# Optimization experiments

Hardware: AMD Instinct MI355X
Metric: run time of the kernel (lower is better)

The kernel has to match this reference:

```python
import jax, jax.numpy as jnp
import numpy as np

THETA = 10000.0
NUM_HEADS = 16


def _rope(x, token_positions):
    # x: [B, H, S, d_k], token_positions: [B, S]
    d_k = x.shape[-1]
    half = d_k // 2
    k = jnp.arange(half, dtype=jnp.float32)
    inv_k = THETA ** (-2.0 * k / d_k)                      # [half]
    pos = token_positions.astype(jnp.float32)              # [B, S]
    angles = pos[..., None] * inv_k                         # [B, S, half]
    angles = jnp.repeat(angles, 2, axis=-1)                 # [B, S, d_k] interleaved
    cos = jnp.cos(angles)[:, None]                          # [B, 1, S, d_k]
    sin = jnp.sin(angles)[:, None]
    x_even = x[..., ::2]
    x_odd = x[..., 1::2]
    r_x = jnp.stack((-x_odd, x_even), axis=-1).reshape(x.shape)
    return x * cos + r_x * sin


def setup_inputs() -> dict:
    key = jax.random.key(0)
    ks = jax.random.split(key, 6)
    B, S, D = 4, 2048, 1024
    delta = 2.0 / np.sqrt(D + D)
    x = jax.random.normal(ks[0], (B, S, D), dtype=jnp.float32)
    Wq = jax.random.normal(ks[1], (D, D), dtype=jnp.float32) * delta
    Wk = jax.random.normal(ks[2], (D, D), dtype=jnp.float32) * delta
    Wv = jax.random.normal(ks[3], (D, D), dtype=jnp.float32) * delta
    Wo = jax.random.normal(ks[4], (D, D), dtype=jnp.float32) * delta
    token_positions = jnp.broadcast_to(jnp.arange(S, dtype=jnp.int64), (B, S))
    return {"x": x, "Wq": Wq, "Wk": Wk, "Wv": Wv, "Wo": Wo,
            "token_positions": token_positions}


def reference(x, Wq, Wk, Wv, Wo, token_positions):
    B, S, D = x.shape
    H = NUM_HEADS
    d_k = D // H

    def split_heads(t):
        return t.reshape(B, S, H, d_k).transpose(0, 2, 1, 3)  # [B, H, S, d_k]

    q = split_heads(x @ Wq.T)
    k = split_heads(x @ Wk.T)
    v = split_heads(x @ Wv.T)

    q = _rope(q, token_positions)
    k = _rope(k, token_positions)

    scores = jnp.einsum('bhqd,bhkd->bhqk', q, k) / jnp.sqrt(jnp.float32(d_k))
    causal = jnp.tril(jnp.ones((S, S), dtype=bool))
    scores = jnp.where(causal, scores, -jnp.inf)
    prob = jax.nn.softmax(scores, axis=-1)
    out = jnp.einsum('bhqk,bhkd->bhqd', prob, v)            # [B, H, S, d_k]
    out = out.transpose(0, 2, 1, 3).reshape(B, S, D)
    return out @ Wo.T
```

## Files before the change

kernel.cpp:

```cpp
#include <hip/hip_runtime.h>
#include <math.h>


typedef __attribute__((ext_vector_type(4))) float f32x4;
typedef __attribute__((ext_vector_type(8))) short bf16x8;
typedef __attribute__((ext_vector_type(4))) short bf16x4;

#define MFMA16(A,B,C) __builtin_amdgcn_mfma_f32_16x16x32_bf16((A),(B),(C),0,0,0)

#if __has_builtin(__builtin_amdgcn_mfma_f32_16x16x16bf16_1k)
#define PV_K16 1
#define MFMA16X16(A,B,C) __builtin_amdgcn_mfma_f32_16x16x16bf16_1k((A),(B),(C),0,0,0)
#endif

__device__ __forceinline__ unsigned short f2b(float f) {
  unsigned int i = __float_as_uint(f);
  unsigned int r = (i + 0x7fffu + ((i >> 16) & 1u)) >> 16;
  return (unsigned short)r;
}
__device__ __forceinline__ float b2f(unsigned short u) {
  return __uint_as_float(((unsigned int)u) << 16);
}
__device__ __forceinline__ unsigned int cvt_pk_bf16(float lo, float hi) {
  unsigned int r;
  asm("v_cvt_pk_bf16_f32 %0, %1, %2" : "=v"(r) : "v"(lo), "v"(hi));
  return r;
}
__device__ __forceinline__ float exp2_fast(float x) {
  float r;
  asm("v_exp_f32 %0, %1" : "=v"(r) : "v"(x));
  return r;
}

__device__ __forceinline__ void gload_lds16(const void* g, void* l) {
  __builtin_amdgcn_global_load_lds((const __attribute__((address_space(1))) void*)g,
                                   (__attribute__((address_space(3))) void*)l,
                                   16, 0, 0);
}

__global__ __launch_bounds__(256) void cvt_kernel(const float* __restrict__ in,
                                                  unsigned short* __restrict__ out,
                                                  int n8) {
  int i = blockIdx.x * 256 + threadIdx.x;
  if (i >= n8) return;
  const float4* p = reinterpret_cast<const float4*>(in) + (size_t)i * 2;
  float4 a = p[0], b = p[1];
  union { unsigned short us[8]; uint4 v; } u;
  u.us[0] = f2b(a.x); u.us[1] = f2b(a.y); u.us[2] = f2b(a.z); u.us[3] = f2b(a.w);
  u.us[4] = f2b(b.x); u.us[5] = f2b(b.y); u.us[6] = f2b(b.z); u.us[7] = f2b(b.w);
  reinterpret_cast<uint4*>(out)[i] = u.v;
}

__global__ __launch_bounds__(256) void cvt_w_kernel(const float* __restrict__ Wq,
                                                    const float* __restrict__ Wk,
                                                    const float* __restrict__ Wv,
                                                    const float* __restrict__ Wo,
                                                    unsigned short* __restrict__ Wcat,
                                                    unsigned short* __restrict__ Wob,
                                                    float2* __restrict__ tab) {
  int i = blockIdx.x * 256 + threadIdx.x;
  if (i < 65536) {
    int pos = i >> 5, k = i & 31;
    float inv = exp2f(-0.41524101f * (float)k);
    float s, c;
    sincosf((float)pos * inv, &s, &c);
    tab[i] = make_float2(c, s);
  }
  int mat = i >> 17;
  int off = i & 131071;
  const float* src = (mat == 0) ? Wq : (mat == 1) ? Wk : (mat == 2) ? Wv : Wo;
  unsigned short* dst = (mat < 3) ? (Wcat + ((size_t)mat << 20)) : Wob;
  const float4* p = reinterpret_cast<const float4*>(src) + (size_t)off * 2;
  float4 a = p[0], b = p[1];
  union { unsigned short us[8]; uint4 v; } u;
  u.us[0] = f2b(a.x); u.us[1] = f2b(a.y); u.us[2] = f2b(a.z); u.us[3] = f2b(a.w);
  u.us[4] = f2b(b.x); u.us[5] = f2b(b.y); u.us[6] = f2b(b.z); u.us[7] = f2b(b.w);
  reinterpret_cast<uint4*>(dst)[off] = u.v;
}

template <int EPI, int NTX>
__global__ __launch_bounds__(256, 2) void gemm_bt64(const unsigned short* __restrict__ A,
                                                    const unsigned short* __restrict__ Bw,
                                                    const float2* __restrict__ tab,
                                                    unsigned short* __restrict__ Dq,
                                                    unsigned short* __restrict__ Dk,
                                                    unsigned short* __restrict__ Dv) {
  __shared__ __attribute__((aligned(16))) short a_lds[2][128 * 64];
  __shared__ __attribute__((aligned(16))) short b_lds[2][128 * 64];
  const int tid  = threadIdx.x;
  const int lane = tid & 63;
  const int wid  = tid >> 6;
  const int lr = lane & 15, lc = lane >> 4;
  const int wr = wid >> 1, wc = wid & 1;

  const int NB = NTX * 64;
  const int id = blockIdx.x;
  const int nid = (id & 7) * (NB / 8) + (id >> 3);
  const int bx = nid % NTX;
  const int by = nid / NTX;
  const int m0 = by * 128;
  const int n0 = bx * 128;

  f32x4 acc[4][4];
#pragma unroll
  for (int i = 0; i < 4; i++)
#pragma unroll
    for (int j = 0; j < 4; j++) acc[i][j] = (f32x4){0.f, 0.f, 0.f, 0.f};

  const int srow = tid >> 3;
  const int sgx  = (tid & 7) ^ (srow & 7);
  const unsigned short* ag = A  + (size_t)(m0 + srow) * 1024 + sgx * 8;
  const unsigned short* bg = Bw + (size_t)(n0 + srow) * 1024 + sgx * 8;

#pragma unroll
  for (int p = 0; p < 4; p++) {
    gload_lds16(ag + p * 32768, &a_lds[0][tid * 8 + p * 2048]);
    gload_lds16(bg + p * 32768, &b_lds[0][tid * 8 + p * 2048]);
  }
  __syncthreads();

  int buf = 0;
  for (int k0 = 0; k0 < 1024; k0 += 64) {
    if (k0 + 64 < 1024) {
      const int nb = buf ^ 1;
#pragma unroll
      for (int p = 0; p < 4; p++) {
        gload_lds16(ag + (k0 + 64) + p * 32768, &a_lds[nb][tid * 8 + p * 2048]);
        gload_lds16(bg + (k0 + 64) + p * 32768, &b_lds[nb][tid * 8 + p * 2048]);
      }
    }
#pragma unroll
    for (int kc = 0; kc < 2; kc++) {
      bf16x8 af[4], bfr[4];
#pragma unroll
      for (int t = 0; t < 4; t++) {
        const int ra = wr * 64 + t * 16 + lr;
        const int rb = wc * 64 + t * 16 + lr;
        af[t]  = *(const bf16x8*)&a_lds[buf][ra * 64 + (((kc * 4 + lc) ^ (ra & 7)) * 8)];
        bfr[t] = *(const bf16x8*)&b_lds[buf][rb * 64 + (((kc * 4 + lc) ^ (rb & 7)) * 8)];
      }
#pragma unroll
      for (int i = 0; i < 4; i++)
#pragma unroll
        for (int j = 0; j < 4; j++) acc[i][j] = MFMA16(af[i], bfr[j], acc[i][j]);
    }
    __syncthreads();
    buf ^= 1;
  }

  if (EPI == 2) {
    float* D = (float*)Dq;
#pragma unroll
    for (int i = 0; i < 4; i++)
#pragma unroll
      for (int j = 0; j < 4; j++)
#pragma unroll
        for (int r = 0; r < 4; r++) {
          int m = m0 + wr * 64 + i * 16 + lc * 4 + r;
          int n = n0 + wc * 64 + j * 16 + lr;
          D[(size_t)m * 1024 + n] = acc[i][j][r];
        }
  } else if (n0 >= 2048) {
#pragma unroll
    for (int i = 0; i < 4; i++)
#pragma unroll
      for (int j = 0; j < 4; j++)
#pragma unroll
        for (int r = 0; r < 4; r++) {
          int m = m0 + wr * 64 + i * 16 + lc * 4 + r;
          int nl = (n0 - 2048) + wc * 64 + j * 16 + lr;
          int b = m >> 11, s = m & 2047;
          int h = nl >> 6, d = nl & 63;
          Dv[((size_t)((b * 16 + h) * 64 + d) << 11) + s] = f2b(acc[i][j][r]);
        }
  } else {
    const bool isQ = (n0 < 1024);
    const float qs = isQ ? 0.18033688011112042f : 1.0f;
    unsigned short* D = isQ ? Dq : Dk;
    const int odd = lane & 1;
#pragma unroll
    for (int j = 0; j < 4; j++) {
      const int i0 = (j * 16 + lr) >> 1;
#pragma unroll
      for (int i = 0; i < 4; i++)
#pragma unroll
        for (int r = 0; r < 4; r++) {
          int m = m0 + wr * 64 + i * 16 + lc * 4 + r;
          int n = n0 + wc * 64 + j * 16 + lr;
          float2 t = tab[(m & 2047) * 32 + i0];
          float v = acc[i][j][r];
          float pv = __shfl_xor(v, 1);
          float res = (v * t.x + (odd ? pv : -pv) * t.y) * qs;
          D[(size_t)m * 1024 + (n & 1023)] = f2b(res);
        }
    }
  }
}

__global__ __launch_bounds__(512, 4) void attn_kernel(const unsigned short* __restrict__ Q,
                                                      const unsigned short* __restrict__ K,
                                                      const unsigned short* __restrict__ Vt,
                                                      unsigned short* __restrict__ O) {
  __shared__ __attribute__((aligned(16))) char K_lds[2][8192];
  __shared__ __attribute__((aligned(16))) char V_lds[2][8192];
#ifndef PV_K16
  __shared__ __attribute__((aligned(16))) short P_lds[8][16][72];
#endif

  const int t    = threadIdx.x;
  const int lane = t & 63;
  const int wid  = t >> 6;
  const int lr = lane & 15, lc = (lane >> 4) & 3;
  const int lc4 = lc * 4;
  const int sbase = lane & 48;
  const int rswz = (lr & 7) << 4;
  const int csw0 = (lc * 16) ^ rswz;
  const int csw1 = (64 + lc * 16) ^ rswz;

  const int id  = blockIdx.y * 8 + blockIdx.x;
  const int nid = (id & 7) * 64 + (id >> 3);
  const int bx  = nid & 7;
  const int bh  = nid >> 3;
  const int b   = bh >> 4;

  const unsigned short* Qb = Q  + (size_t)b * 2048 * 1024 + (bh & 15) * 64;
  const unsigned short* Kb = K  + (size_t)b * 2048 * 1024 + (bh & 15) * 64;
  const unsigned short* Vb = Vt + (size_t)bh * 64 * 2048;

  const int srow = t >> 3;
  const int scol = ((t & 7) * 16) ^ ((srow & 7) << 4);
  const char* kstage = (const char*)Kb + (size_t)srow * 2048 + scol;
  const char* vstage = (const char*)Vb + (size_t)srow * 4096 + scol;
  const int t16 = t * 16;

#ifndef PV_K16
  short* myP = &P_lds[wid][0][0];
#endif

  gload_lds16(kstage, &K_lds[0][t16]);
  gload_lds16(vstage, &V_lds[0][t16]);
  __syncthreads();
  int buf = 0;

  for (int half = 0; half < 2; half++) {
    const int band = half ? (15 - bx) : bx;
    const int n = 2 * band + 2;
    const int qw = band * 128 + wid * 16;

    bf16x8 qf[2];
#pragma unroll
    for (int c = 0; c < 2; c++)
      qf[c] = *(const bf16x8*)(Qb + (size_t)(qw + lr) * 1024 + c * 32 + lc * 8);

    f32x4 acc[4];
#pragma unroll
    for (int d = 0; d < 4; d++) acc[d] = (f32x4){0.f, 0.f, 0.f, 0.f};
    float mrow = -1e30f, lrow = 0.f;

    for (int tt = 0; tt < n; tt++) {
      const int kv0 = tt << 6;

      if (tt + 1 < n) {
        const size_t ko = (size_t)(kv0 + 64);
        gload_lds16(kstage + ko * 2048, &K_lds[buf ^ 1][t16]);
        gload_lds16(vstage + ko * 2,    &V_lds[buf ^ 1][t16]);
      } else if (half == 0) {
        gload_lds16(kstage, &K_lds[buf ^ 1][t16]);
        gload_lds16(vstage, &V_lds[buf ^ 1][t16]);
      }

      const char* kb = K_lds[buf] + lr * 128;

      f32x4 st[4];
      __builtin_amdgcn_s_setprio(1);
#pragma unroll
      for (int nt = 0; nt < 4; nt++) {
        bf16x8 ka0 = *(const bf16x8*)(kb + nt * 2048 + csw0);
        bf16x8 ka1 = *(const bf16x8*)(kb + nt * 2048 + csw1);
        f32x4 s4 = (f32x4){0.f, 0.f, 0.f, 0.f};
        s4 = MFMA16(ka0, qf[0], s4);
        s4 = MFMA16(ka1, qf[1], s4);
        st[nt] = s4;
      }
      __builtin_amdgcn_s_setprio(0);

      if (kv0 + 64 > qw) {
        const int lim = qw + lr - kv0 - lc4;
#pragma unroll
        for (int nt = 0; nt < 4; nt++)
#pragma unroll
          for (int r = 0; r < 4; r++)
            if (nt * 16 + r > lim) st[nt][r] = -1e30f;
      }

      float t0 = fmaxf(fmaxf(st[0][0], st[0][1]), fmaxf(st[0][2], st[0][3]));
      float t1 = fmaxf(fmaxf(st[1][0], st[1][1]), fmaxf(st[1][2], st[1][3]));
      float t2 = fmaxf(fmaxf(st[2][0], st[2][1]), fmaxf(st[2][2], st[2][3]));
      float t3 = fmaxf(fmaxf(st[3][0], st[3][1]), fmaxf(st[3][2], st[3][3]));
      float tm = fmaxf(fmaxf(t0, t1), fmaxf(t2, t3));
      tm = fmaxf(tm, __shfl_xor(tm, 16));
      tm = fmaxf(tm, __shfl_xor(tm, 32));

      const bool grow = !__all(tm <= mrow + 8.0f);
      float scale = 1.0f;
      if (grow) {
        float mnew = fmaxf(mrow, tm);
        scale = exp2_fast(mrow - mnew);
        mrow = mnew;
      }

#pragma unroll
      for (int nt = 0; nt < 4; nt++)
#pragma unroll
        for (int r = 0; r < 4; r++) st[nt][r] = exp2_fast(st[nt][r] - mrow);

      float s0 = (st[0][0] + st[0][1]) + (st[0][2] + st[0][3]);
      float s1 = (st[1][0] + st[1][1]) + (st[1][2] + st[1][3]);
      float s2 = (st[2][0] + st[2][1]) + (st[2][2] + st[2][3]);
      float s3 = (st[3][0] + st[3][1]) + (st[3][2] + st[3][3]);
      float psum = (s0 + s1) + (s2 + s3);
      psum += __shfl_xor(psum, 16);
      psum += __shfl_xor(psum, 32);

      if (grow) {
        lrow *= scale;
        float sc4[4];
#pragma unroll
        for (int r = 0; r < 4; r++) sc4[r] = __shfl(scale, sbase | (lc4 + r));
#pragma unroll
        for (int d = 0; d < 4; d++) {
          acc[d][0] *= sc4[0]; acc[d][1] *= sc4[1];
          acc[d][2] *= sc4[2]; acc[d][3] *= sc4[3];
        }
      }
      lrow += psum;

#ifdef PV_K16
      bf16x4 pfr[4];
#pragma unroll
      for (int nt = 0; nt < 4; nt++) {
        union { uint2 u; bf16x4 v; } pu;
        pu.u.x = cvt_pk_bf16(st[nt][0], st[nt][1]);
        pu.u.y = cvt_pk_bf16(st[nt][2], st[nt][3]);
        pfr[nt] = pu.v;
      }
      const char* vbase = V_lds[buf];
      __builtin_amdgcn_s_setprio(1);
#pragma unroll
      for (int nt = 0; nt < 4; nt++) {
        const int cb = (nt * 32 + lc * 8) ^ rswz;
#pragma unroll
        for (int d = 0; d < 4; d++) {
          bf16x4 vf = *(const bf16x4*)(vbase + (d * 16 + lr) * 128 + cb);
          acc[d] = MFMA16X16(pfr[nt], vf, acc[d]);
        }
      }
      __builtin_amdgcn_s_setprio(0);
#else
#pragma unroll
      for (int nt = 0; nt < 4; nt++) {
        uint2 w;
        w.x = cvt_pk_bf16(st[nt][0], st[nt][1]);
        w.y = cvt_pk_bf16(st[nt][2], st[nt][3]);
        *(uint2*)&myP[lr * 72 + nt * 16 + lc4] = w;
      }
      const char* vb = V_lds[buf] + lr * 128;
      __builtin_amdgcn_s_setprio(1);
#pragma unroll
      for (int c = 0; c < 2; c++) {
        bf16x8 pa = *(const bf16x8*)&myP[lr * 72 + c * 32 + lc * 8];
        const int csw = c ? csw1 : csw0;
#pragma unroll
        for (int d = 0; d < 4; d++) {
          bf16x8 vf = *(const bf16x8*)(vb + d * 2048 + csw);
          acc[d] = MFMA16(pa, vf, acc[d]);
        }
      }
      __builtin_amdgcn_s_setprio(0);
#endif

      __syncthreads();
      buf ^= 1;
    }

    float linv[4];
#pragma unroll
    for (int r = 0; r < 4; r++)
      linv[r] = __builtin_amdgcn_rcpf(__shfl(lrow, sbase | (lc4 + r)));

    const int hcol = (bh & 15) * 64;
#pragma unroll
    for (int d = 0; d < 4; d++)
#pragma unroll
      for (int r = 0; r < 4; r++) {
        int q = qw + lc4 + r;
        O[(size_t)(b * 2048 + q) * 1024 + hcol + d * 16 + lr] = f2b(acc[d][r] * linv[r]);
      }
  }
}

extern "C" void kernel_launch(void* const* d_in, const int* in_sizes, int n_in,
                              void* d_out, int out_size, void* d_ws, size_t ws_size,
                              hipStream_t stream) {
  const float* x  = (const float*)d_in[0];
  const float* Wq = (const float*)d_in[1];
  const float* Wk = (const float*)d_in[2];
  const float* Wv = (const float*)d_in[3];
  const float* Wo = (const float*)d_in[4];
  float* out = (float*)d_out;

  char* ws = (char*)d_ws;
  const size_t MB = 1u << 20;
  unsigned short* xb   = (unsigned short*)(ws);
  unsigned short* Wcat = (unsigned short*)(ws + 16 * MB);
  unsigned short* Wob  = (unsigned short*)(ws + 22 * MB);
  unsigned short* Qb   = (unsigned short*)(ws + 24 * MB);
  unsigned short* Kb   = (unsigned short*)(ws + 40 * MB);
  unsigned short* Vtb  = (unsigned short*)(ws + 56 * MB);
  unsigned short* Ob   = xb;

  float2* tab = (float2*)d_out;

  cvt_kernel<<<4096, 256, 0, stream>>>(x, xb, 1048576);
  cvt_w_kernel<<<2048, 256, 0, stream>>>(Wq, Wk, Wv, Wo, Wcat, Wob, tab);

  gemm_bt64<1, 24><<<1536, 256, 0, stream>>>(xb, Wcat, tab, Qb, Kb, Vtb);

  attn_kernel<<<dim3(8, 64), 512, 0, stream>>>(Qb, Kb, Vtb, Ob);

  gemm_bt64<2, 8><<<512, 256, 0, stream>>>(Ob, Wob, nullptr, (unsigned short*)out, nullptr, nullptr);
}
```

Measured before the change: 168.2 us.

## Double KV tile size per stage to halve barriers in attention loop

The attention loop now stages two 64-row KV tiles per double-buffer slot (128 rows of K and V), processing them as two sub-iterations between each __syncthreads. This halves the number of block-wide barriers and prefetch phases per query band, and the V LDS layout becomes 256-byte rows with an adjusted swizzle. The non-PV_K16 path also drops the P round-trip through LDS and builds the P operand in registers instead. LDS use doubles to 64KB per block, which may limit occupancy. Because band tile counts are always even, the pairing stays exact.

```diff
diff --git a/kernel.cpp b/kernel.cpp
--- a/kernel.cpp
+++ b/kernel.cpp
@@ -201,11 +201,8 @@
                                                       const unsigned short* __restrict__ K,
                                                       const unsigned short* __restrict__ Vt,
                                                       unsigned short* __restrict__ O) {
-  __shared__ __attribute__((aligned(16))) char K_lds[2][8192];
-  __shared__ __attribute__((aligned(16))) char V_lds[2][8192];
-#ifndef PV_K16
-  __shared__ __attribute__((aligned(16))) short P_lds[8][16][72];
-#endif
+  __shared__ __attribute__((aligned(16))) char K_lds[2][16384];
+  __shared__ __attribute__((aligned(16))) char V_lds[2][16384];
 
   const int t    = threadIdx.x;
   const int lane = t & 63;
@@ -227,18 +224,18 @@
   const unsigned short* Kb = K  + (size_t)b * 2048 * 1024 + (bh & 15) * 64;
   const unsigned short* Vb = Vt + (size_t)bh * 64 * 2048;
 
-  const int srow = t >> 3;
-  const int scol = ((t & 7) * 16) ^ ((srow & 7) << 4);
-  const char* kstage = (const char*)Kb + (size_t)srow * 2048 + scol;
-  const char* vstage = (const char*)Vb + (size_t)srow * 4096 + scol;
+  const int srowK = t >> 3;
+  const int scolK = ((t & 7) * 16) ^ ((srowK & 7) << 4);
+  const char* kstage = (const char*)Kb + (size_t)srowK * 2048 + scolK;
+  const int srowV = t >> 4;
+  const int scolV = ((t & 15) * 16) ^ ((srowV & 7) << 4);
+  const char* vstage = (const char*)Vb + (size_t)srowV * 4096 + scolV;
   const int t16 = t * 16;
 
-#ifndef PV_K16
-  short* myP = &P_lds[wid][0][0];
-#endif
-
   gload_lds16(kstage, &K_lds[0][t16]);
+  gload_lds16(kstage + 64 * 2048, &K_lds[0][8192 + t16]);
   gload_lds16(vstage, &V_lds[0][t16]);
+  gload_lds16(vstage + 32 * 4096, &V_lds[0][8192 + t16]);
   __syncthreads();
   int buf = 0;
 
@@ -257,127 +254,136 @@
     for (int d = 0; d < 4; d++) acc[d] = (f32x4){0.f, 0.f, 0.f, 0.f};
     float mrow = -1e30f, lrow = 0.f;
 
-    for (int tt = 0; tt < n; tt++) {
-      const int kv0 = tt << 6;
-
-      if (tt + 1 < n) {
-        const size_t ko = (size_t)(kv0 + 64);
+    for (int tp = 0; tp < n; tp += 2) {
+      if (tp + 2 < n) {
+        const size_t ko = (size_t)(tp + 2) << 6;
         gload_lds16(kstage + ko * 2048, &K_lds[buf ^ 1][t16]);
-        gload_lds16(vstage + ko * 2,    &V_lds[buf ^ 1][t16]);
+        gload_lds16(kstage + (ko + 64) * 2048, &K_lds[buf ^ 1][8192 + t16]);
+        gload_lds16(vstage + ko * 2, &V_lds[buf ^ 1][t16]);
+        gload_lds16(vstage + 32 * 4096 + ko * 2, &V_lds[buf ^ 1][8192 + t16]);
       } else if (half == 0) {
         gload_lds16(kstage, &K_lds[buf ^ 1][t16]);
+        gload_lds16(kstage + 64 * 2048, &K_lds[buf ^ 1][8192 + t16]);
         gload_lds16(vstage, &V_lds[buf ^ 1][t16]);
+        gload_lds16(vstage + 32 * 4096, &V_lds[buf ^ 1][8192 + t16]);
       }
 
-      const char* kb = K_lds[buf] + lr * 128;
-
-      f32x4 st[4];
-      __builtin_amdgcn_s_setprio(1);
-#pragma unroll
-      for (int nt = 0; nt < 4; nt++) {
-        bf16x8 ka0 = *(const bf16x8*)(kb + nt * 2048 + csw0);
-        bf16x8 ka1 = *(const bf16x8*)(kb + nt * 2048 + csw1);
-        f32x4 s4 = (f32x4){0.f, 0.f, 0.f, 0.f};
-        s4 = MFMA16(ka0, qf[0], s4);
-        s4 = MFMA16(ka1, qf[1], s4);
-        st[nt] = s4;
+#pragma unroll
+      for (int sub = 0; sub < 2; sub++) {
+        const int tt = tp + sub;
+        const int kv0 = tt << 6;
+        const char* kb = K_lds[buf] + (sub * 64 + lr) * 128;
+
+        f32x4 st[4];
+        __builtin_amdgcn_s_setprio(1);
+#pragma unroll
+        for (int nt = 0; nt < 4; nt++) {
+          bf16x8 ka0 = *(const bf16x8*)(kb + nt * 2048 + csw0);
+          bf16x8 ka1 = *(const bf16x8*)(kb + nt * 2048 + csw1);
+          f32x4 s4 = (f32x4){0.f, 0.f, 0.f, 0.f};
+          s4 = MFMA16(ka0, qf[0], s4);
+          s4 = MFMA16(ka1, qf[1], s4);
+          st[nt] = s4;
+        }
+        __builtin_amdgcn_s_setprio(0);
+
+        if (kv0 + 64 > qw) {
+          const int lim = qw + lr - kv0 - lc4;
+#pragma unroll
+          for (int nt = 0; nt < 4; nt++)
+#pragma unroll
+            for (int r = 0; r < 4; r++)
+              if (nt * 16 + r > lim) st[nt][r] = -1e30f;
+        }
+
+        float t0 = fmaxf(fmaxf(st[0][0], st[0][1]), fmaxf(st[0][2], st[0][3]));
+        float t1 = fmaxf(fmaxf(st[1][0], st[1][1]), fmaxf(st[1][2], st[1][3]));
+        float t2 = fmaxf(fmaxf(st[2][0], st[2][1]), fmaxf(st[2][2], st[2][3]));
+        float t3 = fmaxf(fmaxf(st[3][0], st[3][1]), fmaxf(st[3][2], st[3][3]));
+        float tm = fmaxf(fmaxf(t0, t1), fmaxf(t2, t3));
+        tm = fmaxf(tm, __shfl_xor(tm, 16));
+        tm = fmaxf(tm, __shfl_xor(tm, 32));
+
+        const bool grow = !__all(tm <= mrow + 8.0f);
+        float scale = 1.0f;
+        if (grow) {
+          float mnew = fmaxf(mrow, tm);
+          scale = exp2_fast(mrow - mnew);
+          mrow = mnew;
+        }
+
+#pragma unroll
+        for (int nt = 0; nt < 4; nt++)
+#pragma unroll
+          for (int r = 0; r < 4; r++) st[nt][r] = exp2_fast(st[nt][r] - mrow);
+
+        float s0 = (st[0][0] + st[0][1]) + (st[0][2] + st[0][3]);
+        float s1 = (st[1][0] + st[1][1]) + (st[1][2] + st[1][3]);
+        float s2 = (st[2][0] + st[2][1]) + (st[2][2] + st[2][3]);
+        float s3 = (st[3][0] + st[3][1]) + (st[3][2] + st[3][3]);
+        float psum = (s0 + s1) + (s2 + s3);
+        psum += __shfl_xor(psum, 16);
+        psum += __shfl_xor(psum, 32);
+
+        if (grow) {
+          lrow *= scale;
+          float sc4[4];
+#pragma unroll
+          for (int r = 0; r < 4; r++) sc4[r] = __shfl(scale, sbase | (lc4 + r));
+#pragma unroll
+          for (int d = 0; d < 4; d++) {
+            acc[d][0] *= sc4[0]; acc[d][1] *= sc4[1];
+            acc[d][2] *= sc4[2]; acc[d][3] *= sc4[3];
+          }
+        }
+        lrow += psum;
+
+#ifdef PV_K16
+        bf16x4 pfr[4];
+#pragma unroll
+        for (int nt = 0; nt < 4; nt++) {
+          union { uint2 u; bf16x4 v; } pu;
+          pu.u.x = cvt_pk_bf16(st[nt][0], st[nt][1]);
+          pu.u.y = cvt_pk_bf16(st[nt][2], st[nt][3]);
+          pfr[nt] = pu.v;
+        }
+        const char* vbase = V_lds[buf];
+        __builtin_amdgcn_s_setprio(1);
+#pragma unroll
+        for (int nt = 0; nt < 4; nt++) {
+          const int cb = (sub * 128 + nt * 32 + lc * 8) ^ rswz;
+#pragma unroll
+          for (int d = 0; d < 4; d++) {
+            bf16x4 vf = *(const bf16x4*)(vbase + (d * 16 + lr) * 256 + cb);
+            acc[d] = MFMA16X16(pfr[nt], vf, acc[d]);
+          }
+        }
+        __builtin_amdgcn_s_setprio(0);
+#else
+        bf16x8 pa[2];
+#pragma unroll
+        for (int c = 0; c < 2; c++) {
+          union { unsigned int u[4]; bf16x8 v; } pu;
+          pu.u[0] = cvt_pk_bf16(st[2 * c][0], st[2 * c][1]);
+          pu.u[1] = cvt_pk_bf16(st[2 * c][2], st[2 * c][3]);
+          pu.u[2] = cvt_pk_bf16(st[2 * c + 1][0], st[2 * c + 1][1]);
+          pu.u[3] = cvt_pk_bf16(st[2 * c + 1][2], st[2 * c + 1][3]);
+          pa[c] = pu.v;
+        }
+        const char* vbase = V_lds[buf];
+        __builtin_amdgcn_s_setprio(1);
+#pragma unroll
+        for (int c = 0; c < 2; c++) {
+          const int cb = (sub * 128 + c * 64 + lc * 16) ^ rswz;
+#pragma unroll
+          for (int d = 0; d < 4; d++) {
+            bf16x8 vf = *(const bf16x8*)(vbase + (d * 16 + lr) * 256 + cb);
+            acc[d] = MFMA16(pa[c], vf, acc[d]);
+          }
+        }
+        __builtin_amdgcn_s_setprio(0);
+#endif
       }
-      __builtin_amdgcn_s_setprio(0);
-
-      if (kv0 + 64 > qw) {
-        const int lim = qw + lr - kv0 - lc4;
-#pragma unroll
-        for (int nt = 0; nt < 4; nt++)
-#pragma unroll
-          for (int r = 0; r < 4; r++)
-            if (nt * 16 + r > lim) st[nt][r] = -1e30f;
-      }
-
-      float t0 = fmaxf(fmaxf(st[0][0], st[0][1]), fmaxf(st[0][2], st[0][3]));
-      float t1 = fmaxf(fmaxf(st[1][0], st[1][1]), fmaxf(st[1][2], st[1][3]));
-      float t2 = fmaxf(fmaxf(st[2][0], st[2][1]), fmaxf(st[2][2], st[2][3]));
-      float t3 = fmaxf(fmaxf(st[3][0], st[3][1]), fmaxf(st[3][2], st[3][3]));
-      float tm = fmaxf(fmaxf(t0, t1), fmaxf(t2, t3));
-      tm = fmaxf(tm, __shfl_xor(tm, 16));
-      tm = fmaxf(tm, __shfl_xor(tm, 32));
-
-      const bool grow = !__all(tm <= mrow + 8.0f);
-      float scale = 1.0f;
-      if (grow) {
-        float mnew = fmaxf(mrow, tm);
-        scale = exp2_fast(mrow - mnew);
-        mrow = mnew;
-      }
-
-#pragma unroll
-      for (int nt = 0; nt < 4; nt++)
-#pragma unroll
-        for (int r = 0; r < 4; r++) st[nt][r] = exp2_fast(st[nt][r] - mrow);
-
-      float s0 = (st[0][0] + st[0][1]) + (st[0][2] + st[0][3]);
-      float s1 = (st[1][0] + st[1][1]) + (st[1][2] + st[1][3]);
-      float s2 = (st[2][0] + st[2][1]) + (st[2][2] + st[2][3]);
-      float s3 = (st[3][0] + st[3][1]) + (st[3][2] + st[3][3]);
-      float psum = (s0 + s1) + (s2 + s3);
-      psum += __shfl_xor(psum, 16);
-      psum += __shfl_xor(psum, 32);
-
-      if (grow) {
-        lrow *= scale;
-        float sc4[4];
-#pragma unroll
-        for (int r = 0; r < 4; r++) sc4[r] = __shfl(scale, sbase | (lc4 + r));
-#pragma unroll
-        for (int d = 0; d < 4; d++) {
-          acc[d][0] *= sc4[0]; acc[d][1] *= sc4[1];
-          acc[d][2] *= sc4[2]; acc[d][3] *= sc4[3];
-        }
-      }
-      lrow += psum;
-
-#ifdef PV_K16
-      bf16x4 pfr[4];
-#pragma unroll
-      for (int nt = 0; nt < 4; nt++) {
-        union { uint2 u; bf16x4 v; } pu;
-        pu.u.x = cvt_pk_bf16(st[nt][0], st[nt][1]);
-        pu.u.y = cvt_pk_bf16(st[nt][2], st[nt][3]);
-        pfr[nt] = pu.v;
-      }
-      const char* vbase = V_lds[buf];
-      __builtin_amdgcn_s_setprio(1);
-#pragma unroll
-      for (int nt = 0; nt < 4; nt++) {
-        const int cb = (nt * 32 + lc * 8) ^ rswz;
-#pragma unroll
-        for (int d = 0; d < 4; d++) {
-          bf16x4 vf = *(const bf16x4*)(vbase + (d * 16 + lr) * 128 + cb);
-          acc[d] = MFMA16X16(pfr[nt], vf, acc[d]);
-        }
-      }
-      __builtin_amdgcn_s_setprio(0);
-#else
-#pragma unroll
-      for (int nt = 0; nt < 4; nt++) {
-        uint2 w;
-        w.x = cvt_pk_bf16(st[nt][0], st[nt][1]);
-        w.y = cvt_pk_bf16(st[nt][2], st[nt][3]);
-        *(uint2*)&myP[lr * 72 + nt * 16 + lc4] = w;
-      }
-      const char* vb = V_lds[buf] + lr * 128;
-      __builtin_amdgcn_s_setprio(1);
-#pragma unroll
-      for (int c = 0; c < 2; c++) {
-        bf16x8 pa = *(const bf16x8*)&myP[lr * 72 + c * 32 + lc * 8];
-        const int csw = c ? csw1 : csw0;
-#pragma unroll
-        for (int d = 0; d < 4; d++) {
-          bf16x8 vf = *(const bf16x8*)(vb + d * 2048 + csw);
-          acc[d] = MFMA16(pa, vf, acc[d]);
-        }
-      }
-      __builtin_amdgcn_s_setprio(0);
-#endif
 
       __syncthreads();
       buf ^= 1;
```

New measurement: 165.4 us (median of 2 runs). About the same (-1.6%).

## Triple-buffer K/V tiles with prefetch depth two in attention kernel

Applied to the files above, without the earlier changes.

Moves the K/V LDS staging from double to triple buffering. Loads now run two tiles ahead across both causal bands, and a partial vmcnt wait plus a raw barrier replaces the full __syncthreads, so global loads overlap more compute. The non-PV_K16 path also packs P into registers in place of an LDS round trip. The cost is 50% more LDS per block, which may reduce occupancy, and extra wrap-around index logic for the combined band schedule.

```diff
diff --git a/kernel.cpp b/kernel.cpp
--- a/kernel.cpp
+++ b/kernel.cpp
@@ -201,11 +201,8 @@
                                                       const unsigned short* __restrict__ K,
                                                       const unsigned short* __restrict__ Vt,
                                                       unsigned short* __restrict__ O) {
-  __shared__ __attribute__((aligned(16))) char K_lds[2][8192];
-  __shared__ __attribute__((aligned(16))) char V_lds[2][8192];
-#ifndef PV_K16
-  __shared__ __attribute__((aligned(16))) short P_lds[8][16][72];
-#endif
+  __shared__ __attribute__((aligned(16))) char K_lds[3][8192];
+  __shared__ __attribute__((aligned(16))) char V_lds[3][8192];
 
   const int t    = threadIdx.x;
   const int lane = t & 63;
@@ -233,19 +230,23 @@
   const char* vstage = (const char*)Vb + (size_t)srow * 4096 + scol;
   const int t16 = t * 16;
 
-#ifndef PV_K16
-  short* myP = &P_lds[wid][0][0];
-#endif
+  const int n0 = 2 * bx + 2;
 
   gload_lds16(kstage, &K_lds[0][t16]);
   gload_lds16(vstage, &V_lds[0][t16]);
-  __syncthreads();
-  int buf = 0;
+  gload_lds16(kstage + 64 * 2048, &K_lds[1][t16]);
+  gload_lds16(vstage + 64 * 2, &V_lds[1][t16]);
+  asm volatile("s_waitcnt vmcnt(2)" ::: "memory");
+  __builtin_amdgcn_s_barrier();
+
+  int sb = 2;
+  int jb = 0;
 
   for (int half = 0; half < 2; half++) {
     const int band = half ? (15 - bx) : bx;
     const int n = 2 * band + 2;
     const int qw = band * 128 + wid * 16;
+    const int ssbase = half ? n0 : 0;
 
     bf16x8 qf[2];
 #pragma unroll
@@ -258,18 +259,17 @@
     float mrow = -1e30f, lrow = 0.f;
 
     for (int tt = 0; tt < n; tt++) {
+      {
+        const int ss = ssbase + tt + 2;
+        const int sv = (ss < 34) ? ss : 0;
+        const int kv = ((sv < n0) ? sv : (sv - n0)) << 6;
+        gload_lds16(kstage + (size_t)kv * 2048, &K_lds[sb][t16]);
+        gload_lds16(vstage + (size_t)kv * 2,    &V_lds[sb][t16]);
+        sb = (sb == 2) ? 0 : sb + 1;
+      }
+
       const int kv0 = tt << 6;
-
-      if (tt + 1 < n) {
-        const size_t ko = (size_t)(kv0 + 64);
-        gload_lds16(kstage + ko * 2048, &K_lds[buf ^ 1][t16]);
-        gload_lds16(vstage + ko * 2,    &V_lds[buf ^ 1][t16]);
-      } else if (half == 0) {
-        gload_lds16(kstage, &K_lds[buf ^ 1][t16]);
-        gload_lds16(vstage, &V_lds[buf ^ 1][t16]);
-      }
-
-      const char* kb = K_lds[buf] + lr * 128;
+      const char* kb = K_lds[jb] + lr * 128;
 
       f32x4 st[4];
       __builtin_amdgcn_s_setprio(1);
@@ -344,7 +344,7 @@
         pu.u.y = cvt_pk_bf16(st[nt][2], st[nt][3]);
         pfr[nt] = pu.v;
       }
-      const char* vbase = V_lds[buf];
+      const char* vbase = V_lds[jb];
       __builtin_amdgcn_s_setprio(1);
 #pragma unroll
       for (int nt = 0; nt < 4; nt++) {
@@ -357,30 +357,33 @@
       }
       __builtin_amdgcn_s_setprio(0);
 #else
-#pragma unroll
-      for (int nt = 0; nt < 4; nt++) {
-        uint2 w;
-        w.x = cvt_pk_bf16(st[nt][0], st[nt][1]);
-        w.y = cvt_pk_bf16(st[nt][2], st[nt][3]);
-        *(uint2*)&myP[lr * 72 + nt * 16 + lc4] = w;
-      }
-      const char* vb = V_lds[buf] + lr * 128;
+      bf16x8 pa[2];
+#pragma unroll
+      for (int c = 0; c < 2; c++) {
+        union { unsigned int u[4]; bf16x8 v; } pu;
+        pu.u[0] = cvt_pk_bf16(st[2 * c][0], st[2 * c][1]);
+        pu.u[1] = cvt_pk_bf16(st[2 * c][2], st[2 * c][3]);
+        pu.u[2] = cvt_pk_bf16(st[2 * c + 1][0], st[2 * c + 1][1]);
+        pu.u[3] = cvt_pk_bf16(st[2 * c + 1][2], st[2 * c + 1][3]);
+        pa[c] = pu.v;
+      }
+      const char* vbase = V_lds[jb];
       __builtin_amdgcn_s_setprio(1);
 #pragma unroll
       for (int c = 0; c < 2; c++) {
-        bf16x8 pa = *(const bf16x8*)&myP[lr * 72 + c * 32 + lc * 8];
-        const int csw = c ? csw1 : csw0;
+        const int cb = (c * 64 + lc * 16) ^ rswz;
 #pragma unroll
         for (int d = 0; d < 4; d++) {
-          bf16x8 vf = *(const bf16x8*)(vb + d * 2048 + csw);
-          acc[d] = MFMA16(pa, vf, acc[d]);
+          bf16x8 vf = *(const bf16x8*)(vbase + (d * 16 + lr) * 128 + cb);
+          acc[d] = MFMA16(pa[c], vf, acc[d]);
         }
       }
       __builtin_amdgcn_s_setprio(0);
 #endif
 
-      __syncthreads();
-      buf ^= 1;
+      asm volatile("s_waitcnt vmcnt(2)" ::: "memory");
+      __builtin_amdgcn_s_barrier();
+      jb = (jb == 2) ? 0 : jb + 1;
     }
 
     float linv[4];
```

Measured after the change: 168.2 us. No clear change (+0.0%).
